# Kernel optimization log

Measured on AMD Instinct MI355X. Metric: run time of the kernel, lower is better.

Reference implementation:

```python
import jax, jax.numpy as jnp
import numpy as np

IN_F = 4096
OUT_F = 4096
N_TOK = 8192
MAX_ITER = IN_F * OUT_F // 2  # default max_iter=-1 -> half of weight entries


def _approx_matmul(x, weight, max_iter):
    """Budgeted approximate matmul: only the `max_iter` largest-magnitude
    weight entries participate (the rest of the multiply-accumulate budget is
    skipped). Faithful to the iteration-budget semantics of Approx_Matmul:
    max_iter multiply-adds out of in_features*out_features total.
    """
    n = weight.size
    flat_abs = jnp.abs(weight).reshape(-1)
    # threshold = k-th largest magnitude (static k -> jit-friendly)
    kth = jnp.sort(flat_abs)[n - max_iter]
    mask = (jnp.abs(weight) >= kth).astype(weight.dtype)
    w_eff = weight * jax.lax.stop_gradient(mask)
    # y[t, o] = sum_i x[t, i] * w_eff[o, i]
    return jnp.einsum('ti,oi->to', x, w_eff)


def setup_inputs() -> dict:
    key = jax.random.key(0)
    kx, kw, kb = jax.random.split(key, 3)
    x = jax.random.normal(kx, (N_TOK, IN_F), dtype=jnp.float32)
    # kaiming_uniform_(a=sqrt(5)) on [out, in] -> bound = 1/sqrt(in_features)
    bound = 1.0 / np.sqrt(IN_F)
    weight = jax.random.uniform(kw, (OUT_F, IN_F), dtype=jnp.float32,
                                minval=-bound, maxval=bound)
    bias = jax.random.uniform(kb, (OUT_F,), dtype=jnp.float32,
                              minval=-bound, maxval=bound)
    return {"x": x, "weight": weight, "bias": bias}


def reference(x, weight, bias):
    mid = _approx_matmul(x, weight, MAX_ITER)
    return mid + bias
```

## Files before the change

kernel.cpp:

```cpp
#include <hip/hip_runtime.h>

#define IN_F   4096
#define OUT_F  4096
#define N_TOK  8192
#define NW     (OUT_F * IN_F)
#define SEL_TARGET 8388608u
#define CAND_CAP (1u << 20)

#define LO_BITS 0x3BFCA000u
#define HI_BITS 0x3C018000u

typedef unsigned int  u32;
typedef unsigned short u16;

typedef __bf16 bf16x8 __attribute__((ext_vector_type(8)));
typedef float  f32x4  __attribute__((ext_vector_type(4)));
typedef u32    u32x4  __attribute__((ext_vector_type(4)));

__device__ inline u16 f2bf_rne(float f) {
    u32 u = __float_as_uint(f);
    u32 r = (u + 0x7fffu + ((u >> 16) & 1u)) >> 16;
    return (u16)r;
}

__global__ __launch_bounds__(256) void scanw_kernel(
    const uint4* __restrict__ wb, u16* __restrict__ w16,
    u32* __restrict__ cand, u32* __restrict__ cpos,
    u32* __restrict__ scal) {
    __shared__ u32 lbuf[4096];
    __shared__ u32 lpos[4096];
    __shared__ u32 lcnt, gbase, lblw;
    if (threadIdx.x == 0) { lcnt = 0; lblw = 0; }
    __syncthreads();

    const int base = blockIdx.x * 4096;
    u32 cntb = 0;
    #pragma unroll 4
    for (int j = 0; j < 16; j++) {
        const int vi = base + threadIdx.x + j * 256;
        uint4 v = wb[vi];
        u32 r[4] = {v.x, v.y, v.z, v.w};
        ushort4 o;
        u16* op = (u16*)&o;
        #pragma unroll
        for (int e = 0; e < 4; e++) {
            u32 kk = r[e] & 0x7fffffffu;
            cntb += (kk < LO_BITS) ? 1u : 0u;
            op[e] = (kk >= LO_BITS) ? f2bf_rne(__uint_as_float(r[e])) : (u16)0;
            if (kk >= LO_BITS && kk < HI_BITS) {
                u32 idx = atomicAdd(&lcnt, 1u);
                if (idx < 4096) { lbuf[idx] = kk; lpos[idx] = (u32)vi * 4u + e; }
                else scal[6] = 1u;
            }
        }
        *(ushort4*)&w16[(size_t)vi * 4] = o;
    }
    #pragma unroll
    for (int off = 32; off; off >>= 1) cntb += __shfl_down(cntb, off);
    if ((threadIdx.x & 63) == 0) atomicAdd(&lblw, cntb);
    __syncthreads();
    if (threadIdx.x == 0) {
        gbase = atomicAdd(&scal[3], min(lcnt, 4096u));
        atomicAdd(&scal[4], lblw);
    }
    __syncthreads();
    const u32 n = min(lcnt, 4096u), gb = gbase;
    for (u32 i = threadIdx.x; i < n; i += 256)
        if (gb + i < CAND_CAP) { cand[gb + i] = lbuf[i]; cpos[gb + i] = lpos[i]; }
}

#define SCAN1024(part, t)                                            \
    do { _Pragma("unroll")                                           \
        for (int off_ = 1; off_ < 1024; off_ <<= 1) {                \
            u32 v_ = ((t) >= off_) ? part[(t) - off_] : 0u;          \
            __syncthreads();                                         \
            part[t] += v_;                                           \
            __syncthreads();                                         \
        } } while (0)

__global__ __launch_bounds__(1024) void mid_kernel(const u32* __restrict__ cand,
                                                   const uint4* __restrict__ wb,
                                                   const f32x4* __restrict__ xb,
                                                   u16* __restrict__ x16,
                                                   u32* __restrict__ scal) {
    if (blockIdx.x != 0) {
        const int stride = 2048 * 1024;
        for (int i = (blockIdx.x - 1) * 1024 + threadIdx.x;
             i < (N_TOK * IN_F) / 4; i += stride) {
            f32x4 v = __builtin_nontemporal_load(&xb[i]);
            ushort4 o;
            o.x = f2bf_rne(v.x);
            o.y = f2bf_rne(v.y);
            o.z = f2bf_rne(v.z);
            o.w = f2bf_rne(v.w);
            *(ushort4*)&x16[(size_t)i * 4] = o;
        }
        return;
    }

    __shared__ u32 h[2048];
    __shared__ u32 part[1024];
    __shared__ u32 sh[2];
    const int t = threadIdx.x;
    const u32 n = scal[3], below = scal[4], ovf = scal[6];
    const bool valid = (n > 0) && (n <= CAND_CAP) && (ovf == 0) &&
                       (below <= SEL_TARGET) && (SEL_TARGET < below + n);

    if (valid) {
        u32 tgt = SEL_TARGET - below;
        const uint4* c4 = (const uint4*)cand;
        const u32 n4 = n >> 2;

        h[t] = 0; h[t + 1024] = 0;
        __syncthreads();
        for (u32 i = t; i < n4; i += 1024) {
            uint4 v = c4[i];
            atomicAdd(&h[(v.x - LO_BITS) >> 9], 1u);
            atomicAdd(&h[(v.y - LO_BITS) >> 9], 1u);
            atomicAdd(&h[(v.z - LO_BITS) >> 9], 1u);
            atomicAdd(&h[(v.w - LO_BITS) >> 9], 1u);
        }
        for (u32 i = (n4 << 2) + t; i < n; i += 1024)
            atomicAdd(&h[(cand[i] - LO_BITS) >> 9], 1u);
        __syncthreads();
        u32 c = h[t];
        part[t] = c;
        __syncthreads();
        SCAN1024(part, t);
        u32 cum = (t == 0) ? 0u : part[t - 1];
        if (tgt >= cum && tgt < cum + c) { sh[0] = (u32)t; sh[1] = tgt - cum; }
        __syncthreads();
        const u32 b1 = sh[0];
        tgt = sh[1];
        __syncthreads();

        h[t] = 0; h[t + 1024] = 0;
        __syncthreads();
        for (u32 i = t; i < n4; i += 1024) {
            uint4 v = c4[i];
            u32 d0 = v.x - LO_BITS, d1 = v.y - LO_BITS,
                d2 = v.z - LO_BITS, d3 = v.w - LO_BITS;
            if ((d0 >> 9) == b1) atomicAdd(&h[d0 & 511u], 1u);
            if ((d1 >> 9) == b1) atomicAdd(&h[d1 & 511u], 1u);
            if ((d2 >> 9) == b1) atomicAdd(&h[d2 & 511u], 1u);
            if ((d3 >> 9) == b1) atomicAdd(&h[d3 & 511u], 1u);
        }
        for (u32 i = (n4 << 2) + t; i < n; i += 1024) {
            u32 d = cand[i] - LO_BITS;
            if ((d >> 9) == b1) atomicAdd(&h[d & 511u], 1u);
        }
        __syncthreads();
        c = (t < 512) ? h[t] : 0u;
        part[t] = c;
        __syncthreads();
        SCAN1024(part, t);
        cum = (t == 0) ? 0u : part[t - 1];
        if (tgt >= cum && tgt < cum + c)
            scal[2] = LO_BITS + (b1 << 9) + (u32)t;
        return;
    }

    if (t == 0) scal[7] = 1u;
    u32 tgt = SEL_TARGET;
    const int nvec = NW / 4;
    h[t] = 0; h[t + 1024] = 0;
    __syncthreads();
    for (int i = t; i < nvec; i += 1024) {
        uint4 v = wb[i];
        atomicAdd(&h[(v.x & 0x7fffffffu) >> 20], 1u);
        atomicAdd(&h[(v.y & 0x7fffffffu) >> 20], 1u);
        atomicAdd(&h[(v.z & 0x7fffffffu) >> 20], 1u);
        atomicAdd(&h[(v.w & 0x7fffffffu) >> 20], 1u);
    }
    __syncthreads();
    u32 a0 = h[2 * t], a1 = h[2 * t + 1];
    part[t] = a0 + a1;
    __syncthreads();
    SCAN1024(part, t);
    u32 cum = (t == 0) ? 0u : part[t - 1];
    if (tgt >= cum && tgt < cum + a0) { sh[0] = (u32)(2 * t);     sh[1] = tgt - cum; }
    cum += a0;
    if (tgt >= cum && tgt < cum + a1) { sh[0] = (u32)(2 * t + 1); sh[1] = tgt - cum; }
    __syncthreads();
    const u32 b1f = sh[0];
    tgt = sh[1];
    __syncthreads();

    h[t] = 0; h[t + 1024] = 0;
    __syncthreads();
    for (int i = t; i < nvec; i += 1024) {
        uint4 v = wb[i];
        u32 k[4] = {v.x & 0x7fffffffu, v.y & 0x7fffffffu,
                    v.z & 0x7fffffffu, v.w & 0x7fffffffu};
        #pragma unroll
        for (int e = 0; e < 4; e++)
            if ((k[e] >> 20) == b1f) atomicAdd(&h[(k[e] >> 9) & 2047u], 1u);
    }
    __syncthreads();
    a0 = h[2 * t]; a1 = h[2 * t + 1];
    part[t] = a0 + a1;
    __syncthreads();
    SCAN1024(part, t);
    cum = (t == 0) ? 0u : part[t - 1];
    if (tgt >= cum && tgt < cum + a0) { sh[0] = (u32)(2 * t);     sh[1] = tgt - cum; }
    cum += a0;
    if (tgt >= cum && tgt < cum + a1) { sh[0] = (u32)(2 * t + 1); sh[1] = tgt - cum; }
    __syncthreads();
    const u32 pfx22 = (b1f << 11) | sh[0];
    tgt = sh[1];
    __syncthreads();

    h[t] = 0; h[t + 1024] = 0;
    __syncthreads();
    for (int i = t; i < nvec; i += 1024) {
        uint4 v = wb[i];
        u32 k[4] = {v.x & 0x7fffffffu, v.y & 0x7fffffffu,
                    v.z & 0x7fffffffu, v.w & 0x7fffffffu};
        #pragma unroll
        for (int e = 0; e < 4; e++)
            if ((k[e] >> 9) == pfx22) atomicAdd(&h[k[e] & 511u], 1u);
    }
    __syncthreads();
    u32 c = (t < 512) ? h[t] : 0u;
    part[t] = c;
    __syncthreads();
    SCAN1024(part, t);
    cum = (t == 0) ? 0u : part[t - 1];
    if (tgt >= cum && tgt < cum + c)
        scal[2] = (pfx22 << 9) | (u32)t;
}

__global__ __launch_bounds__(256) void finalize_w_kernel(
    const u32* __restrict__ cand, const u32* __restrict__ cpos,
    const u32x4* __restrict__ wb, u16* __restrict__ w16,
    const u32* __restrict__ scal) {
    const u32 kth = scal[2];
    const u32 stride = gridDim.x * blockDim.x;
    if (scal[7] == 1u) {
        const u32 nvec = NW / 4;
        for (u32 i = blockIdx.x * blockDim.x + threadIdx.x; i < nvec; i += stride) {
            u32x4 v = __builtin_nontemporal_load(&wb[i]);
            ushort4 o;
            o.x = ((v.x & 0x7fffffffu) >= kth) ? f2bf_rne(__uint_as_float(v.x)) : (u16)0;
            o.y = ((v.y & 0x7fffffffu) >= kth) ? f2bf_rne(__uint_as_float(v.y)) : (u16)0;
            o.z = ((v.z & 0x7fffffffu) >= kth) ? f2bf_rne(__uint_as_float(v.z)) : (u16)0;
            o.w = ((v.w & 0x7fffffffu) >= kth) ? f2bf_rne(__uint_as_float(v.w)) : (u16)0;
            *(ushort4*)&w16[(size_t)i * 4] = o;
        }
    } else {
        const u32 n = min(scal[3], CAND_CAP);
        for (u32 i = blockIdx.x * blockDim.x + threadIdx.x; i < n; i += stride)
            if (cand[i] < kth) w16[cpos[i]] = (u16)0;
    }
}

#define BK 64
#define NT (IN_F / BK)

#define ASLOT(buf, ks) (((buf) * 2 + (ks)) * 8192)
#define BSLOT(buf, ks) (32768 + ((buf) * 2 + (ks)) * 8192)
#define KOFF(kt, ks)   ((kt) * BK + (ks) * 32)

#define VMCNT(n) asm volatile("s_waitcnt vmcnt(" #n ")" ::: "memory")
#define LGKM0    asm volatile("s_waitcnt lgkmcnt(0)" ::: "memory")
#define BARR()   __builtin_amdgcn_s_barrier()

__global__ __launch_bounds__(512, 2) void gemm8p(
    const u16* __restrict__ A,
    const u16* __restrict__ B,
    const float* __restrict__ bias,
    float* __restrict__ C) {
    __shared__ u16 lds[65536];

    const int tid  = threadIdx.x;
    const int lane = tid & 63;
    const int ln15 = lane & 15;
    const int l16  = lane >> 4;
    const int wv   = tid >> 6;
    const int wr   = wv >> 2;
    const int wc   = wv & 3;
    const int wrow = wr * 128;
    const int wcol = wc * 64;

    const int bid = blockIdx.x;
    const int xcd = bid & 7;
    const int j   = bid >> 3;
    const int by  = xcd * 4 + (j & 3);
    const int bx  = j >> 2;
    const int arow = by * 256;
    const int brow = bx * 256;

    const int q0 = tid,       r0 = q0 >> 2, c0 = (q0 & 3) ^ ((r0 >> 1) & 3);
    const int q1 = tid + 512, r1 = q1 >> 2, c1 = (q1 & 3) ^ ((r1 >> 1) & 3);
    const u16* pA0 = A + (size_t)(arow + r0) * IN_F + c0 * 8;
    const u16* pA1 = A + (size_t)(arow + r1) * IN_F + c1 * 8;
    const u16* pB0 = B + (size_t)(brow + r0) * IN_F + c0 * 8;
    const u16* pB1 = B + (size_t)(brow + r1) * IN_F + c1 * 8;

    f32x4 acc[8][4];
    #pragma unroll
    for (int m = 0; m < 8; m++)
        #pragma unroll
        for (int n = 0; n < 4; n++)
            acc[m][n] = {0.f, 0.f, 0.f, 0.f};

    #define STAGE2(p0, p1, koff, slot) do {                                             \
        __builtin_amdgcn_global_load_lds(                                               \
            (const __attribute__((address_space(1))) unsigned int*)((p0) + (koff)),     \
            (__attribute__((address_space(3))) unsigned int*)&lds[(slot) + tid * 8],    \
            16, 0, 0);                                                                  \
        __builtin_amdgcn_global_load_lds(                                               \
            (const __attribute__((address_space(1))) unsigned int*)((p1) + (koff)),     \
            (__attribute__((address_space(3))) unsigned int*)&lds[(slot) + (tid + 512) * 8], \
            16, 0, 0);                                                                  \
    } while (0)

    #define READ_A(mh, ks, buf) do {                                                    \
        _Pragma("unroll")                                                               \
        for (int i_ = 0; i_ < 4; i_++) {                                                \
            int row_ = wrow + ((mh) * 4 + i_) * 16 + ln15;                              \
            int cc_  = l16 ^ ((row_ >> 1) & 3);                                         \
            aF[i_] = *(const bf16x8*)&lds[ASLOT(buf, ks) + row_ * 32 + cc_ * 8];        \
        } } while (0)

    #define READ_B(ks, buf) do {                                                       \
        _Pragma("unroll")                                                               \
        for (int i_ = 0; i_ < 4; i_++) {                                                \
            int row_ = wcol + i_ * 16 + ln15;                                           \
            int cc_  = l16 ^ ((row_ >> 1) & 3);                                         \
            bF[i_] = *(const bf16x8*)&lds[BSLOT(buf, ks) + row_ * 32 + cc_ * 8];        \
        } } while (0)

    #define MFMAQ(mh) do {                                                              \
        __builtin_amdgcn_s_setprio(1);                                                  \
        _Pragma("unroll")                                                               \
        for (int i_ = 0; i_ < 4; i_++)                                                  \
            _Pragma("unroll")                                                           \
            for (int n_ = 0; n_ < 4; n_++)                                              \
                acc[(mh) * 4 + i_][n_] = __builtin_amdgcn_mfma_f32_16x16x32_bf16(       \
                    aF[i_], bF[n_], acc[(mh) * 4 + i_][n_], 0, 0, 0);                   \
        __builtin_amdgcn_s_setprio(0);                                                  \
    } while (0)

    STAGE2(pB0, pB1, KOFF(0, 0), BSLOT(0, 0));
    STAGE2(pA0, pA1, KOFF(0, 0), ASLOT(0, 0));
    STAGE2(pB0, pB1, KOFF(0, 1), BSLOT(0, 1));
    STAGE2(pA0, pA1, KOFF(0, 1), ASLOT(0, 1));
    VMCNT(4);
    STAGE2(pB0, pB1, KOFF(1, 0), BSLOT(1, 0));
    STAGE2(pA0, pA1, KOFF(1, 0), ASLOT(1, 0));
    STAGE2(pB0, pB1, KOFF(1, 1), BSLOT(1, 1));
    VMCNT(6);
    BARR();

    bf16x8 aF[4], bF[4];

    #pragma unroll 1
    for (int it = 0; it < NT / 2; it++) {
        const int t0 = 2 * it;
        const int ka = t0 + 1;
        const int kb = min(t0 + 2, NT - 1);
        const int kc = min(t0 + 3, NT - 1);

        READ_A(0, 0, 0); READ_B(0, 0);
        STAGE2(pA0, pA1, KOFF(ka, 1), ASLOT(1, 1));
        BARR(); LGKM0; MFMAQ(0); BARR();
        READ_A(1, 0, 0);
        STAGE2(pB0, pB1, KOFF(kb, 0), BSLOT(0, 0));
        BARR(); LGKM0; MFMAQ(1); BARR();
        READ_A(0, 1, 0); READ_B(1, 0);
        STAGE2(pA0, pA1, KOFF(kb, 0), ASLOT(0, 0));
        BARR(); LGKM0; MFMAQ(0); BARR();
        READ_A(1, 1, 0);
        STAGE2(pB0, pB1, KOFF(kb, 1), BSLOT(0, 1));
        VMCNT(6);
        BARR(); LGKM0; MFMAQ(1); BARR();

        READ_A(0, 0, 1); READ_B(0, 1);
        STAGE2(pA0, pA1, KOFF(kb, 1), ASLOT(0, 1));
        BARR(); LGKM0; MFMAQ(0); BARR();
        READ_A(1, 0, 1);
        STAGE2(pB0, pB1, KOFF(kc, 0), BSLOT(1, 0));
        BARR(); LGKM0; MFMAQ(1); BARR();
        READ_A(0, 1, 1); READ_B(1, 1);
        STAGE2(pA0, pA1, KOFF(kc, 0), ASLOT(1, 0));
        BARR(); LGKM0; MFMAQ(0); BARR();
        READ_A(1, 1, 1);
        STAGE2(pB0, pB1, KOFF(kc, 1), BSLOT(1, 1));
        VMCNT(6);
        BARR(); LGKM0; MFMAQ(1); BARR();
    }
    VMCNT(0);

    const int cr = l16 * 4;
    #pragma unroll
    for (int n = 0; n < 4; n++) {
        int col = brow + wcol + n * 16 + ln15;
        float bv = bias[col];
        #pragma unroll
        for (int m = 0; m < 8; m++) {
            int rr0 = arow + wrow + m * 16 + cr;
            #pragma unroll
            for (int j2 = 0; j2 < 4; j2++) {
                float vv = acc[m][n][j2] + bv;
                __builtin_nontemporal_store(vv, &C[(size_t)(rr0 + j2) * OUT_F + col]);
            }
        }
    }
}

extern "C" void kernel_launch(void* const* d_in, const int* in_sizes, int n_in,
                              void* d_out, int out_size, void* d_ws, size_t ws_size,
                              hipStream_t stream) {
    const float* x    = (const float*)d_in[0];
    const float* w    = (const float*)d_in[1];
    const float* bias = (const float*)d_in[2];
    float* out = (float*)d_out;

    char* ws = (char*)d_ws;
    u32* scal  = (u32*)(ws + 0);
    u16* w16   = (u16*)(ws + 65536);
    u16* x16   = (u16*)(ws + 65536 + (size_t)NW * 2);
    u32* cand  = (u32*)out;
    u32* cpos  = cand + CAND_CAP;

    hipMemsetAsync(scal, 0, 64, stream);

    scanw_kernel<<<1024, 256, 0, stream>>>((const uint4*)w, w16, cand, cpos, scal);
    mid_kernel<<<2049, 1024, 0, stream>>>(cand, (const uint4*)w, (const f32x4*)x,
                                          x16, scal);
    finalize_w_kernel<<<2048, 256, 0, stream>>>(cand, cpos, (const u32x4*)w,
                                                w16, scal);

    gemm8p<<<512, 512, 0, stream>>>(x16, w16, bias, out);
}
```

Baseline: 333.5 us.

## Process two output tiles per GEMM block, prefetching the next tile during the epilogue

After: 326.7 us. 2.0% less time.

```diff
diff --git a/kernel.cpp b/kernel.cpp
--- a/kernel.cpp
+++ b/kernel.cpp
@@ -285,15 +285,16 @@
     const int bid = blockIdx.x;
     const int xcd = bid & 7;
     const int j   = bid >> 3;
-    const int by  = xcd * 4 + (j & 3);
-    const int bx  = j >> 2;
-    const int arow = by * 256;
+    const int bx  = j >> 1;
+    const int mm  = j & 1;
+    const int by0 = xcd * 4 + mm * 2;
     const int brow = bx * 256;
+    const int arow0 = by0 * 256;
 
     const int q0 = tid,       r0 = q0 >> 2, c0 = (q0 & 3) ^ ((r0 >> 1) & 3);
     const int q1 = tid + 512, r1 = q1 >> 2, c1 = (q1 & 3) ^ ((r1 >> 1) & 3);
-    const u16* pA0 = A + (size_t)(arow + r0) * IN_F + c0 * 8;
-    const u16* pA1 = A + (size_t)(arow + r1) * IN_F + c1 * 8;
+    const u16* pA0 = A + (size_t)(arow0 + r0) * IN_F + c0 * 8;
+    const u16* pA1 = A + (size_t)(arow0 + r1) * IN_F + c1 * 8;
     const u16* pB0 = B + (size_t)(brow + r0) * IN_F + c0 * 8;
     const u16* pB1 = B + (size_t)(brow + r1) * IN_F + c1 * 8;
 
@@ -342,69 +343,92 @@
         __builtin_amdgcn_s_setprio(0);                                                  \
     } while (0)
 
-    STAGE2(pB0, pB1, KOFF(0, 0), BSLOT(0, 0));
-    STAGE2(pA0, pA1, KOFF(0, 0), ASLOT(0, 0));
-    STAGE2(pB0, pB1, KOFF(0, 1), BSLOT(0, 1));
-    STAGE2(pA0, pA1, KOFF(0, 1), ASLOT(0, 1));
-    VMCNT(4);
-    STAGE2(pB0, pB1, KOFF(1, 0), BSLOT(1, 0));
-    STAGE2(pA0, pA1, KOFF(1, 0), ASLOT(1, 0));
-    STAGE2(pB0, pB1, KOFF(1, 1), BSLOT(1, 1));
+    #define PROLOG7() do {                                                              \
+        STAGE2(pB0, pB1, KOFF(0, 0), BSLOT(0, 0));                                      \
+        STAGE2(pA0, pA1, KOFF(0, 0), ASLOT(0, 0));                                      \
+        STAGE2(pB0, pB1, KOFF(0, 1), BSLOT(0, 1));                                      \
+        STAGE2(pA0, pA1, KOFF(0, 1), ASLOT(0, 1));                                      \
+        STAGE2(pB0, pB1, KOFF(1, 0), BSLOT(1, 0));                                      \
+        STAGE2(pA0, pA1, KOFF(1, 0), ASLOT(1, 0));                                      \
+        STAGE2(pB0, pB1, KOFF(1, 1), BSLOT(1, 1));                                      \
+    } while (0)
+
+    PROLOG7();
     VMCNT(6);
     BARR();
 
     bf16x8 aF[4], bF[4];
 
     #pragma unroll 1
-    for (int it = 0; it < NT / 2; it++) {
-        const int t0 = 2 * it;
-        const int ka = t0 + 1;
-        const int kb = min(t0 + 2, NT - 1);
-        const int kc = min(t0 + 3, NT - 1);
-
-        READ_A(0, 0, 0); READ_B(0, 0);
-        STAGE2(pA0, pA1, KOFF(ka, 1), ASLOT(1, 1));
-        BARR(); LGKM0; MFMAQ(0); BARR();
-        READ_A(1, 0, 0);
-        STAGE2(pB0, pB1, KOFF(kb, 0), BSLOT(0, 0));
-        BARR(); LGKM0; MFMAQ(1); BARR();
-        READ_A(0, 1, 0); READ_B(1, 0);
-        STAGE2(pA0, pA1, KOFF(kb, 0), ASLOT(0, 0));
-        BARR(); LGKM0; MFMAQ(0); BARR();
-        READ_A(1, 1, 0);
-        STAGE2(pB0, pB1, KOFF(kb, 1), BSLOT(0, 1));
-        VMCNT(6);
-        BARR(); LGKM0; MFMAQ(1); BARR();
-
-        READ_A(0, 0, 1); READ_B(0, 1);
-        STAGE2(pA0, pA1, KOFF(kb, 1), ASLOT(0, 1));
-        BARR(); LGKM0; MFMAQ(0); BARR();
-        READ_A(1, 0, 1);
-        STAGE2(pB0, pB1, KOFF(kc, 0), BSLOT(1, 0));
-        BARR(); LGKM0; MFMAQ(1); BARR();
-        READ_A(0, 1, 1); READ_B(1, 1);
-        STAGE2(pA0, pA1, KOFF(kc, 0), ASLOT(1, 0));
-        BARR(); LGKM0; MFMAQ(0); BARR();
-        READ_A(1, 1, 1);
-        STAGE2(pB0, pB1, KOFF(kc, 1), BSLOT(1, 1));
-        VMCNT(6);
-        BARR(); LGKM0; MFMAQ(1); BARR();
-    }
-    VMCNT(0);
-
-    const int cr = l16 * 4;
-    #pragma unroll
-    for (int n = 0; n < 4; n++) {
-        int col = brow + wcol + n * 16 + ln15;
-        float bv = bias[col];
+    for (int tile = 0; tile < 2; ++tile) {
+        #pragma unroll 1
+        for (int it = 0; it < NT / 2; it++) {
+            const int t0 = 2 * it;
+            const int ka = t0 + 1;
+            const int kb = min(t0 + 2, NT - 1);
+            const int kc = min(t0 + 3, NT - 1);
+
+            READ_A(0, 0, 0); READ_B(0, 0);
+            STAGE2(pA0, pA1, KOFF(ka, 1), ASLOT(1, 1));
+            BARR(); LGKM0; MFMAQ(0); BARR();
+            READ_A(1, 0, 0);
+            STAGE2(pB0, pB1, KOFF(kb, 0), BSLOT(0, 0));
+            BARR(); LGKM0; MFMAQ(1); BARR();
+            READ_A(0, 1, 0); READ_B(1, 0);
+            STAGE2(pA0, pA1, KOFF(kb, 0), ASLOT(0, 0));
+            BARR(); LGKM0; MFMAQ(0); BARR();
+            READ_A(1, 1, 0);
+            STAGE2(pB0, pB1, KOFF(kb, 1), BSLOT(0, 1));
+            VMCNT(6);
+            BARR(); LGKM0; MFMAQ(1); BARR();
+
+            READ_A(0, 0, 1); READ_B(0, 1);
+            STAGE2(pA0, pA1, KOFF(kb, 1), ASLOT(0, 1));
+            BARR(); LGKM0; MFMAQ(0); BARR();
+            READ_A(1, 0, 1);
+            STAGE2(pB0, pB1, KOFF(kc, 0), BSLOT(1, 0));
+            BARR(); LGKM0; MFMAQ(1); BARR();
+            READ_A(0, 1, 1); READ_B(1, 1);
+            STAGE2(pA0, pA1, KOFF(kc, 0), ASLOT(1, 0));
+            BARR(); LGKM0; MFMAQ(0); BARR();
+            READ_A(1, 1, 1);
+            STAGE2(pB0, pB1, KOFF(kc, 1), BSLOT(1, 1));
+            VMCNT(6);
+            BARR(); LGKM0; MFMAQ(1); BARR();
+        }
+        VMCNT(0);
+
+        if (tile == 0) {
+            pA0 += (size_t)256 * IN_F;
+            pA1 += (size_t)256 * IN_F;
+            PROLOG7();
+        }
+
+        const int arowt = arow0 + tile * 256;
+        const int cr = l16 * 4;
         #pragma unroll
-        for (int m = 0; m < 8; m++) {
-            int rr0 = arow + wrow + m * 16 + cr;
+        for (int n = 0; n < 4; n++) {
+            int col = brow + wcol + n * 16 + ln15;
+            float bv = bias[col];
             #pragma unroll
-            for (int j2 = 0; j2 < 4; j2++) {
-                float vv = acc[m][n][j2] + bv;
-                __builtin_nontemporal_store(vv, &C[(size_t)(rr0 + j2) * OUT_F + col]);
+            for (int m = 0; m < 8; m++) {
+                int rr0 = arowt + wrow + m * 16 + cr;
+                #pragma unroll
+                for (int j2 = 0; j2 < 4; j2++) {
+                    float vv = acc[m][n][j2] + bv;
+                    __builtin_nontemporal_store(vv, &C[(size_t)(rr0 + j2) * OUT_F + col]);
+                }
             }
+        }
+
+        if (tile == 0) {
+            #pragma unroll
+            for (int m = 0; m < 8; m++)
+                #pragma unroll
+                for (int n = 0; n < 4; n++)
+                    acc[m][n] = {0.f, 0.f, 0.f, 0.f};
+            VMCNT(6);
+            BARR();
         }
     }
 }
@@ -432,5 +456,5 @@
     finalize_w_kernel<<<2048, 256, 0, stream>>>(cand, cpos, (const u32x4*)w,
                                                 w16, scal);
 
-    gemm8p<<<512, 512, 0, stream>>>(x16, w16, bias, out);
-}
+    gemm8p<<<256, 512, 0, stream>>>(x16, w16, bias, out);
+}
```
